# Kernel tuning notes

Measured on AMD Instinct MI355X. Metric: run time of the kernel, lower is better.

The kernel has to match this reference:

```python
import jax, jax.numpy as jnp
import numpy as np

N_USERS = 200000
N_ITEMS = 100000
N_EDGES = 1000000
D = 64
NUM_LAYERS = 3
BATCH = 8192


def setup_inputs() -> dict:
    key = jax.random.key(0)
    ks = jax.random.split(key, 8)
    return {
        "user_feat": jax.random.normal(ks[0], (N_USERS, D), dtype=jnp.float32) * 0.1,
        "item_feat": jax.random.normal(ks[1], (N_ITEMS, D), dtype=jnp.float32) * 0.1,
        "edge_u": jax.random.randint(ks[2], (N_EDGES,), 0, N_USERS, dtype=jnp.int32),
        "edge_i": jax.random.randint(ks[3], (N_EDGES,), 0, N_ITEMS, dtype=jnp.int32),
        "norm": jax.random.uniform(ks[4], (N_EDGES,), dtype=jnp.float32),
        "users": jax.random.randint(ks[5], (BATCH,), 0, N_USERS, dtype=jnp.int32),
        "pos_items": jax.random.randint(ks[6], (BATCH,), 0, N_ITEMS, dtype=jnp.int32),
        "neg_items": jax.random.randint(ks[7], (BATCH,), 0, N_ITEMS, dtype=jnp.int32),
    }


def reference(user_feat, item_feat, edge_u, edge_i, norm, users, pos_items, neg_items):
    # LightGCN propagation: each layer does edge-weighted gather-scatter
    # (u_mul_e 'h','norm' -> sum) in both directions of the bipartite graph.
    u_h, i_h = user_feat, item_feat
    u_acc, i_acc = u_h, i_h
    w = norm[:, None]  # [E, 1]
    for _ in range(NUM_LAYERS):
        # user -> item messages
        new_i = jax.ops.segment_sum(u_h[edge_u] * w, edge_i, num_segments=N_ITEMS)
        # item -> user messages
        new_u = jax.ops.segment_sum(i_h[edge_i] * w, edge_u, num_segments=N_USERS)
        u_h, i_h = new_u, new_i
        u_acc = u_acc + u_h
        i_acc = i_acc + i_h
    scale = 1.0 / (NUM_LAYERS + 1)
    u_acc = u_acc * scale
    i_acc = i_acc * scale
    return (u_acc[users], i_acc[pos_items], i_acc[neg_items])
```

## Files before the change

### kernel.cpp

```cpp
#include <hip/hip_runtime.h>


#define N_USERS 200000
#define N_ITEMS 100000
#define N_EDGES 1000000
#define DIM 64
#define BATCH 8192
#define NTOT (N_USERS + N_ITEMS)
#define NOUT (3 * BATCH)
#define NPART 293
#define PLOCAL 1024

#define HA 489
#define NUNITS (NTOT * DIM / 8)
#define CB ((NUNITS + 1023) / 1024)
#define OB (NOUT * 8 / 256)
#define AB8 (NTOT / 32)
#define FB ((NOUT + 255) / 256)

__device__ __forceinline__ unsigned f2bf(float f) {
    unsigned u = __float_as_uint(f);
    return (u + 0x7fffu + ((u >> 16) & 1u)) >> 16;
}
__device__ __forceinline__ uint2 pack4(float4 v) {
    uint2 o;
    o.x = f2bf(v.x) | (f2bf(v.y) << 16);
    o.y = f2bf(v.z) | (f2bf(v.w) << 16);
    return o;
}
__device__ __forceinline__ void fma4(float4& a, uint2 v, float w) {
    a.x += __uint_as_float(v.x << 16) * w;
    a.y += __uint_as_float(v.x & 0xffff0000u) * w;
    a.z += __uint_as_float(v.y << 16) * w;
    a.w += __uint_as_float(v.y & 0xffff0000u) * w;
}
__device__ __forceinline__ int out_bucket(int orow, const int* users,
                                          const int* pos, const int* neg) {
    int seg = orow >> 13;
    int b = orow & (BATCH - 1);
    if (seg == 0) return users[b];
    if (seg == 1) return N_USERS + pos[b];
    return N_USERS + neg[b];
}

__global__ void hist_kernel(const int* __restrict__ eu,
                            const int* __restrict__ ei,
                            int* __restrict__ partTotals)
{
    __shared__ int lh[NPART];
    int bid = blockIdx.x;
    for (int k = threadIdx.x; k < NPART; k += 256) lh[k] = 0;
    __syncthreads();
    int e0 = (bid * 256 + threadIdx.x) * 8;
    if (e0 < N_EDGES) {
        int4 u0 = *reinterpret_cast<const int4*>(eu + e0);
        int4 u1 = *reinterpret_cast<const int4*>(eu + e0 + 4);
        int4 i0 = *reinterpret_cast<const int4*>(ei + e0);
        int4 i1 = *reinterpret_cast<const int4*>(ei + e0 + 4);
        atomicAdd(&lh[u0.x >> 10], 1);
        atomicAdd(&lh[u0.y >> 10], 1);
        atomicAdd(&lh[u0.z >> 10], 1);
        atomicAdd(&lh[u0.w >> 10], 1);
        atomicAdd(&lh[u1.x >> 10], 1);
        atomicAdd(&lh[u1.y >> 10], 1);
        atomicAdd(&lh[u1.z >> 10], 1);
        atomicAdd(&lh[u1.w >> 10], 1);
        atomicAdd(&lh[(N_USERS + i0.x) >> 10], 1);
        atomicAdd(&lh[(N_USERS + i0.y) >> 10], 1);
        atomicAdd(&lh[(N_USERS + i0.z) >> 10], 1);
        atomicAdd(&lh[(N_USERS + i0.w) >> 10], 1);
        atomicAdd(&lh[(N_USERS + i1.x) >> 10], 1);
        atomicAdd(&lh[(N_USERS + i1.y) >> 10], 1);
        atomicAdd(&lh[(N_USERS + i1.z) >> 10], 1);
        atomicAdd(&lh[(N_USERS + i1.w) >> 10], 1);
    }
    __syncthreads();
    for (int k = threadIdx.x; k < NPART; k += 256) {
        int v = lh[k];
        if (v) atomicAdd(&partTotals[k], v);
    }
}

__global__ void part_scan_kernel(const int* __restrict__ partTotals,
                                 int* __restrict__ partStart,
                                 int* __restrict__ gcur)
{
    __shared__ int s[512];
    int t = threadIdx.x;
    s[t] = (t < NPART) ? partTotals[t] : 0;
    __syncthreads();
    for (int off = 1; off < 512; off <<= 1) {
        int x = (t >= off) ? s[t - off] : 0;
        __syncthreads();
        s[t] += x;
        __syncthreads();
    }
    if (t < NPART) {
        int st = (t == 0) ? 0 : s[t - 1];
        partStart[t] = st;
        gcur[t] = st;
    }
    if (t == NPART) partStart[NPART] = s[NPART - 1];
}

__global__ void partition_conv_kernel(const int* __restrict__ eu,
                                      const int* __restrict__ ei,
                                      const float* __restrict__ w,
                                      int* __restrict__ gcur,
                                      uint2* __restrict__ partBuf,
                                      const float4* __restrict__ uf4,
                                      const float4* __restrict__ if4,
                                      unsigned short* __restrict__ F0,
                                      const float* __restrict__ u_feat,
                                      const float* __restrict__ i_feat,
                                      const int* __restrict__ users,
                                      const int* __restrict__ pos,
                                      const int* __restrict__ neg,
                                      float* __restrict__ out)
{
    int bid = blockIdx.x, t = threadIdx.x;
    if (bid < HA) {
        __shared__ int lh[NPART];
        __shared__ int lcur[NPART];
        for (int k = t; k < NPART; k += 256) lh[k] = 0;
        __syncthreads();
        int e0 = (bid * 256 + t) * 8;
        bool act = e0 < N_EDGES;
        int4 u0, u1, i0, i1;
        if (act) {
            u0 = *reinterpret_cast<const int4*>(eu + e0);
            u1 = *reinterpret_cast<const int4*>(eu + e0 + 4);
            i0 = *reinterpret_cast<const int4*>(ei + e0);
            i1 = *reinterpret_cast<const int4*>(ei + e0 + 4);
            atomicAdd(&lh[u0.x >> 10], 1);
            atomicAdd(&lh[u0.y >> 10], 1);
            atomicAdd(&lh[u0.z >> 10], 1);
            atomicAdd(&lh[u0.w >> 10], 1);
            atomicAdd(&lh[u1.x >> 10], 1);
            atomicAdd(&lh[u1.y >> 10], 1);
            atomicAdd(&lh[u1.z >> 10], 1);
            atomicAdd(&lh[u1.w >> 10], 1);
            atomicAdd(&lh[(N_USERS + i0.x) >> 10], 1);
            atomicAdd(&lh[(N_USERS + i0.y) >> 10], 1);
            atomicAdd(&lh[(N_USERS + i0.z) >> 10], 1);
            atomicAdd(&lh[(N_USERS + i0.w) >> 10], 1);
            atomicAdd(&lh[(N_USERS + i1.x) >> 10], 1);
            atomicAdd(&lh[(N_USERS + i1.y) >> 10], 1);
            atomicAdd(&lh[(N_USERS + i1.z) >> 10], 1);
            atomicAdd(&lh[(N_USERS + i1.w) >> 10], 1);
        }
        __syncthreads();
        for (int k = t; k < NPART; k += 256) {
            int v = lh[k];
            lcur[k] = v ? atomicAdd(&gcur[k], v) : 0;
        }
        __syncthreads();
        if (act) {
            float4 wa = *reinterpret_cast<const float4*>(w + e0);
            float4 wb = *reinterpret_cast<const float4*>(w + e0 + 4);
            int us[8] = {u0.x, u0.y, u0.z, u0.w, u1.x, u1.y, u1.z, u1.w};
            int is[8] = {i0.x, i0.y, i0.z, i0.w, i1.x, i1.y, i1.z, i1.w};
            float ws[8] = {wa.x, wa.y, wa.z, wa.w, wb.x, wb.y, wb.z, wb.w};
            #pragma unroll
            for (int j = 0; j < 8; ++j) {
                int bu = us[j];
                int bi = N_USERS + is[j];
                unsigned wbits = __float_as_uint(ws[j]);
                int su = atomicAdd(&lcur[bu >> 10], 1);
                partBuf[su] = make_uint2((unsigned)(bu & 1023) | ((unsigned)bi << 10), wbits);
                int si = atomicAdd(&lcur[bi >> 10], 1);
                partBuf[si] = make_uint2((unsigned)(bi & 1023) | ((unsigned)bu << 10), wbits);
            }
        }
    } else if (bid < HA + CB) {
        const int NU4 = N_USERS * DIM / 4;
        int jb = (bid - HA) * 1024 + t;
        float4 a[4], b[4];
        #pragma unroll
        for (int c = 0; c < 4; ++c) {
            int j = jb + c * 256;
            if (j < NUNITS) {
                int f4 = j * 2;
                if (f4 < NU4) { a[c] = uf4[f4];       b[c] = uf4[f4 + 1]; }
                else          { a[c] = if4[f4 - NU4]; b[c] = if4[f4 - NU4 + 1]; }
            }
        }
        #pragma unroll
        for (int c = 0; c < 4; ++c) {
            int j = jb + c * 256;
            if (j < NUNITS) {
                uint2 pa = pack4(a[c]), pb = pack4(b[c]);
                *reinterpret_cast<uint4*>(F0 + (size_t)j * 8) =
                    make_uint4(pa.x, pa.y, pb.x, pb.y);
            }
        }
    } else {
        int idx = (bid - HA - CB) * 256 + t;
        int row = idx >> 3;
        if (row >= NOUT) return;
        int d8 = (idx & 7) << 3;
        int seg = row >> 13;
        int b = row & (BATCH - 1);
        const float* src;
        if (seg == 0)      src = u_feat + (size_t)users[b] * DIM;
        else if (seg == 1) src = i_feat + (size_t)pos[b]   * DIM;
        else               src = i_feat + (size_t)neg[b]   * DIM;
        float4 v0 = *reinterpret_cast<const float4*>(src + d8);
        float4 v1 = *reinterpret_cast<const float4*>(src + d8 + 4);
        v0.x *= 0.25f; v0.y *= 0.25f; v0.z *= 0.25f; v0.w *= 0.25f;
        v1.x *= 0.25f; v1.y *= 0.25f; v1.z *= 0.25f; v1.w *= 0.25f;
        float* op = out + (size_t)row * DIM + d8;
        *reinterpret_cast<float4*>(op) = v0;
        *reinterpret_cast<float4*>(op + 4) = v1;
    }
}

__global__ void __launch_bounds__(1024)
build_csr_kernel(const int* __restrict__ partStart,
                 const uint2* __restrict__ partBuf,
                 int* __restrict__ rp,
                 int2* __restrict__ entries)
{
    __shared__ int h[PLOCAL];
    __shared__ int s[PLOCAL];
    __shared__ int cur[PLOCAL];
    int p = blockIdx.x, t = threadIdx.x;
    int base = partStart[p], end = partStart[p + 1];
    h[t] = 0;
    __syncthreads();
    for (int r = base + t; r < end; r += 1024)
        atomicAdd(&h[partBuf[r].x & 1023], 1);
    __syncthreads();
    s[t] = h[t];
    __syncthreads();
    for (int off = 1; off < 1024; off <<= 1) {
        int x = (t >= off) ? s[t - off] : 0;
        __syncthreads();
        s[t] += x;
        __syncthreads();
    }
    int c0 = base + s[t] - h[t];
    cur[t] = c0;
    int gb = p * PLOCAL + t;
    if (gb <= NTOT) rp[gb] = c0;
    __syncthreads();
    for (int r = base + t; r < end; r += 1024) {
        uint2 rec = partBuf[r];
        int slot = atomicAdd(&cur[rec.x & 1023], 1);
        entries[slot] = make_int2((int)(rec.x >> 10), (int)rec.y);
    }
}

__device__ __forceinline__ void agg_row8(int row, int l8, int gb,
                                         const int* __restrict__ rp,
                                         const int2* __restrict__ entries,
                                         const unsigned short* __restrict__ src,
                                         float4& sL, float4& sH)
{
    int beg = rp[row], cnt = rp[row + 1] - beg;
    float4 a0L = {0,0,0,0}, a0H = {0,0,0,0}, a1L = {0,0,0,0}, a1H = {0,0,0,0};
    for (int base = 0; base < cnt; base += 8) {
        int2 e = make_int2(0, 0);
        if (base + l8 < cnt) e = entries[beg + base + l8];
        int   c[8];
        float wv[8];
        #pragma unroll
        for (int k = 0; k < 8; ++k) {
            c[k]  = __shfl(e.x, gb + k);
            wv[k] = __int_as_float(__shfl(e.y, gb + k));
        }
        uint4 v[8];
        #pragma unroll
        for (int k = 0; k < 8; ++k)
            v[k] = *reinterpret_cast<const uint4*>(
                src + (size_t)c[k] * DIM + l8 * 8);
        #pragma unroll
        for (int k = 0; k < 8; ++k) {
            if (k & 1) {
                fma4(a1L, make_uint2(v[k].x, v[k].y), wv[k]);
                fma4(a1H, make_uint2(v[k].z, v[k].w), wv[k]);
            } else {
                fma4(a0L, make_uint2(v[k].x, v[k].y), wv[k]);
                fma4(a0H, make_uint2(v[k].z, v[k].w), wv[k]);
            }
        }
    }
    sL.x = a0L.x + a1L.x; sL.y = a0L.y + a1L.y;
    sL.z = a0L.z + a1L.z; sL.w = a0L.w + a1L.w;
    sH.x = a0H.x + a1H.x; sH.y = a0H.y + a1H.y;
    sH.z = a0H.z + a1H.z; sH.w = a0H.w + a1H.w;
}

__global__ void __launch_bounds__(256, 2)
agg1_flag_kernel(const int* __restrict__ rp,
                 const int2* __restrict__ entries,
                 const unsigned short* __restrict__ F0,
                 unsigned short* __restrict__ H1,
                 const int* __restrict__ users,
                 const int* __restrict__ pos,
                 const int* __restrict__ neg,
                 int* __restrict__ flags)
{
    int bid = blockIdx.x;
    if (bid < AB8) {
        int gid = bid * 256 + threadIdx.x;
        int lane = gid & 63;
        int l8 = lane & 7;
        int gb = lane & 56;
        int row = gid >> 3;
        if (row >= NTOT) return;
        float4 sL, sH;
        agg_row8(row, l8, gb, rp, entries, F0, sL, sH);
        uint2 pL = pack4(sL), pH = pack4(sH);
        *reinterpret_cast<uint4*>(H1 + (size_t)row * DIM + l8 * 8) =
            make_uint4(pL.x, pL.y, pH.x, pH.y);
    } else {
        int t = (bid - AB8) * 256 + threadIdx.x;
        if (t >= NOUT) return;
        int bucket = out_bucket(t, users, pos, neg);
        flags[bucket] = 1;
        int beg = rp[bucket], end = rp[bucket + 1];
        for (int k = beg; k < end; ++k)
            flags[entries[k].x] = 1;
    }
}

__global__ void compact_kernel(const int* __restrict__ flags,
                               int* __restrict__ list,
                               int* __restrict__ count)
{
    int t = blockIdx.x * blockDim.x + threadIdx.x;
    int idx = t * 4;
    if (idx >= NTOT) return;
    int4 f = *reinterpret_cast<const int4*>(flags + idx);
    int loc[4]; int k = 0;
    if (f.x) loc[k++] = idx;
    if (f.y) loc[k++] = idx + 1;
    if (f.z) loc[k++] = idx + 2;
    if (f.w) loc[k++] = idx + 3;
    if (k) {
        int base = atomicAdd(count, k);
        for (int m = 0; m < k; ++m) list[base + m] = loc[m];
    }
}

__global__ void __launch_bounds__(256, 2)
agg2_add1_kernel(const int* __restrict__ rp,
                 const int2* __restrict__ entries,
                 const unsigned short* __restrict__ H1,
                 unsigned short* __restrict__ H2,
                 const int* __restrict__ list,
                 const int* __restrict__ count,
                 const int* __restrict__ users,
                 const int* __restrict__ pos,
                 const int* __restrict__ neg,
                 float* __restrict__ out)
{
    int bid = blockIdx.x;
    if (bid < AB8) {
        int gid = bid * 256 + threadIdx.x;
        int lane = gid & 63;
        int l8 = lane & 7;
        int gb = lane & 56;
        int idx = gid >> 3;
        int n = *count;
        if (idx >= n) return;
        int row = list[idx];
        float4 sL, sH;
        agg_row8(row, l8, gb, rp, entries, H1, sL, sH);
        uint2 pL = pack4(sL), pH = pack4(sH);
        *reinterpret_cast<uint4*>(H2 + (size_t)row * DIM + l8 * 8) =
            make_uint4(pL.x, pL.y, pH.x, pH.y);
    } else {
        int idx = (bid - AB8) * 256 + threadIdx.x;
        int row = idx >> 3;
        if (row >= NOUT) return;
        int d8 = (idx & 7) << 3;
        int bucket = out_bucket(row, users, pos, neg);
        uint4 v = *reinterpret_cast<const uint4*>(H1 + (size_t)bucket * DIM + d8);
        float* op = out + (size_t)row * DIM + d8;
        float4 o0 = *reinterpret_cast<const float4*>(op);
        float4 o1 = *reinterpret_cast<const float4*>(op + 4);
        o0.x += 0.25f * __uint_as_float(v.x << 16);
        o0.y += 0.25f * __uint_as_float(v.x & 0xffff0000u);
        o0.z += 0.25f * __uint_as_float(v.y << 16);
        o0.w += 0.25f * __uint_as_float(v.y & 0xffff0000u);
        o1.x += 0.25f * __uint_as_float(v.z << 16);
        o1.y += 0.25f * __uint_as_float(v.z & 0xffff0000u);
        o1.z += 0.25f * __uint_as_float(v.w << 16);
        o1.w += 0.25f * __uint_as_float(v.w & 0xffff0000u);
        *reinterpret_cast<float4*>(op) = o0;
        *reinterpret_cast<float4*>(op + 4) = o1;
    }
}

__global__ void __launch_bounds__(256, 2)
aggout_add2_kernel(const int* __restrict__ rp,
                   const int2* __restrict__ entries,
                   const unsigned short* __restrict__ H2,
                   const int* __restrict__ users,
                   const int* __restrict__ pos,
                   const int* __restrict__ neg,
                   float* __restrict__ out)
{
    int gid = blockIdx.x * 256 + threadIdx.x;
    int lane = gid & 63;
    int l8 = lane & 7;
    int gb = lane & 56;
    int orow = gid >> 3;
    if (orow >= NOUT) return;
    int bucket = out_bucket(orow, users, pos, neg);
    float4 sL, sH;
    agg_row8(bucket, l8, gb, rp, entries, H2, sL, sH);
    uint4 v = *reinterpret_cast<const uint4*>(H2 + (size_t)bucket * DIM + l8 * 8);
    sL.x += __uint_as_float(v.x << 16);
    sL.y += __uint_as_float(v.x & 0xffff0000u);
    sL.z += __uint_as_float(v.y << 16);
    sL.w += __uint_as_float(v.y & 0xffff0000u);
    sH.x += __uint_as_float(v.z << 16);
    sH.y += __uint_as_float(v.z & 0xffff0000u);
    sH.z += __uint_as_float(v.w << 16);
    sH.w += __uint_as_float(v.w & 0xffff0000u);
    float* op = out + (size_t)orow * DIM + l8 * 8;
    float4 o0 = *reinterpret_cast<const float4*>(op);
    float4 o1 = *reinterpret_cast<const float4*>(op + 4);
    o0.x += 0.25f * sL.x; o0.y += 0.25f * sL.y;
    o0.z += 0.25f * sL.z; o0.w += 0.25f * sL.w;
    o1.x += 0.25f * sH.x; o1.y += 0.25f * sH.y;
    o1.z += 0.25f * sH.z; o1.w += 0.25f * sH.w;
    *reinterpret_cast<float4*>(op) = o0;
    *reinterpret_cast<float4*>(op + 4) = o1;
}

extern "C" void kernel_launch(void* const* d_in, const int* in_sizes, int n_in,
                              void* d_out, int out_size, void* d_ws, size_t ws_size,
                              hipStream_t stream)
{
    const float* user_feat = (const float*)d_in[0];
    const float* item_feat = (const float*)d_in[1];
    const int*   eu        = (const int*)d_in[2];
    const int*   ei        = (const int*)d_in[3];
    const float* norm      = (const float*)d_in[4];
    const int*   users     = (const int*)d_in[5];
    const int*   pos       = (const int*)d_in[6];
    const int*   neg       = (const int*)d_in[7];
    float* out = (float*)d_out;

    auto align256 = [](size_t x) { return (x + 255) & ~(size_t)255; };
    const size_t hBytes = (size_t)NTOT * DIM * sizeof(unsigned short);

    char* p = (char*)d_ws;
    unsigned short* F0 = (unsigned short*)p; p += align256(hBytes);
    unsigned short* H1 = (unsigned short*)p; p += align256(hBytes);
    unsigned short* H2 = (unsigned short*)p; p += align256(hBytes);
    int* partTotals = (int*)p; p += align256((size_t)(512 + NTOT + 16) * 4);
    int* flags = partTotals + 512;
    int* count = flags + NTOT;
    int*  partStart = (int*)p;  p += align256(512 * 4);
    int*  gcur      = (int*)p;  p += align256(512 * 4);
    int*  rp        = (int*)p;  p += align256((size_t)(NTOT + 1) * 4);
    uint2* partBuf  = (uint2*)p; p += align256((size_t)2 * N_EDGES * 8);
    int*  list      = (int*)p;  p += align256((size_t)NTOT * 4);
    int2* entries   = (int2*)p; p += align256((size_t)2 * N_EDGES * 8);

    hipMemsetAsync(partTotals, 0, (size_t)(512 + NTOT + 16) * 4, stream);

    hist_kernel<<<HA, 256, 0, stream>>>(eu, ei, partTotals);

    part_scan_kernel<<<1, 512, 0, stream>>>(partTotals, partStart, gcur);

    partition_conv_kernel<<<HA + CB + OB, 256, 0, stream>>>(
        eu, ei, norm, gcur, partBuf,
        (const float4*)user_feat, (const float4*)item_feat, F0,
        user_feat, item_feat, users, pos, neg, out);

    build_csr_kernel<<<NPART, 1024, 0, stream>>>(partStart, partBuf, rp, entries);

    agg1_flag_kernel<<<AB8 + FB, 256, 0, stream>>>(
        rp, entries, F0, H1, users, pos, neg, flags);

    compact_kernel<<<(NTOT / 4 + 255) / 256, 256, 0, stream>>>(flags, list, count);

    agg2_add1_kernel<<<AB8 + OB, 256, 0, stream>>>(
        rp, entries, H1, H2, list, count, users, pos, neg, out);

    aggout_add2_kernel<<<NOUT / 32, 256, 0, stream>>>(
        rp, entries, H2, users, pos, neg, out);
}
```

Baseline: 284.0 us.

## Replace histogram+scan with fixed-capacity partition buckets and nontemporal stores

Removes the histogram and partition-scan kernels by giving each of the 293 partitions a fixed-capacity slot region (CAP entries) in the partition buffer, so edges are bucketed directly with per-partition counters starting at zero. Row pointers become (start,count) int2 pairs, so each row needs one load instead of two. Streaming outputs (F0, H1, H2, partBuf, entries) now use nontemporal stores to avoid polluting cache, and launch_bounds hints are dropped. The fixed capacity assumes no partition exceeds CAP entries for these inputs, which is a correctness risk for skewed graphs, and it enlarges the workspace footprint.

After: 398.6 us. 1.4x slower.

```diff
diff --git a/kernel.cpp b/kernel.cpp
--- a/kernel.cpp
+++ b/kernel.cpp
@@ -10,6 +10,7 @@
 #define NOUT (3 * BATCH)
 #define NPART 293
 #define PLOCAL 1024
+#define CAP 11264
 
 #define HA 489
 #define NUNITS (NTOT * DIM / 8)
@@ -17,6 +18,10 @@
 #define OB (NOUT * 8 / 256)
 #define AB8 (NTOT / 32)
 #define FB ((NOUT + 255) / 256)
+
+typedef int      int2v  __attribute__((ext_vector_type(2)));
+typedef unsigned uint2v __attribute__((ext_vector_type(2)));
+typedef unsigned uint4v __attribute__((ext_vector_type(4)));
 
 __device__ __forceinline__ unsigned f2bf(float f) {
     unsigned u = __float_as_uint(f);
@@ -41,66 +46,6 @@
     if (seg == 0) return users[b];
     if (seg == 1) return N_USERS + pos[b];
     return N_USERS + neg[b];
-}
-
-__global__ void hist_kernel(const int* __restrict__ eu,
-                            const int* __restrict__ ei,
-                            int* __restrict__ partTotals)
-{
-    __shared__ int lh[NPART];
-    int bid = blockIdx.x;
-    for (int k = threadIdx.x; k < NPART; k += 256) lh[k] = 0;
-    __syncthreads();
-    int e0 = (bid * 256 + threadIdx.x) * 8;
-    if (e0 < N_EDGES) {
-        int4 u0 = *reinterpret_cast<const int4*>(eu + e0);
-        int4 u1 = *reinterpret_cast<const int4*>(eu + e0 + 4);
-        int4 i0 = *reinterpret_cast<const int4*>(ei + e0);
-        int4 i1 = *reinterpret_cast<const int4*>(ei + e0 + 4);
-        atomicAdd(&lh[u0.x >> 10], 1);
-        atomicAdd(&lh[u0.y >> 10], 1);
-        atomicAdd(&lh[u0.z >> 10], 1);
-        atomicAdd(&lh[u0.w >> 10], 1);
-        atomicAdd(&lh[u1.x >> 10], 1);
-        atomicAdd(&lh[u1.y >> 10], 1);
-        atomicAdd(&lh[u1.z >> 10], 1);
-        atomicAdd(&lh[u1.w >> 10], 1);
-        atomicAdd(&lh[(N_USERS + i0.x) >> 10], 1);
-        atomicAdd(&lh[(N_USERS + i0.y) >> 10], 1);
-        atomicAdd(&lh[(N_USERS + i0.z) >> 10], 1);
-        atomicAdd(&lh[(N_USERS + i0.w) >> 10], 1);
-        atomicAdd(&lh[(N_USERS + i1.x) >> 10], 1);
-        atomicAdd(&lh[(N_USERS + i1.y) >> 10], 1);
-        atomicAdd(&lh[(N_USERS + i1.z) >> 10], 1);
-        atomicAdd(&lh[(N_USERS + i1.w) >> 10], 1);
-    }
-    __syncthreads();
-    for (int k = threadIdx.x; k < NPART; k += 256) {
-        int v = lh[k];
-        if (v) atomicAdd(&partTotals[k], v);
-    }
-}
-
-__global__ void part_scan_kernel(const int* __restrict__ partTotals,
-                                 int* __restrict__ partStart,
-                                 int* __restrict__ gcur)
-{
-    __shared__ int s[512];
-    int t = threadIdx.x;
-    s[t] = (t < NPART) ? partTotals[t] : 0;
-    __syncthreads();
-    for (int off = 1; off < 512; off <<= 1) {
-        int x = (t >= off) ? s[t - off] : 0;
-        __syncthreads();
-        s[t] += x;
-        __syncthreads();
-    }
-    if (t < NPART) {
-        int st = (t == 0) ? 0 : s[t - 1];
-        partStart[t] = st;
-        gcur[t] = st;
-    }
-    if (t == NPART) partStart[NPART] = s[NPART - 1];
 }
 
 __global__ void partition_conv_kernel(const int* __restrict__ eu,
@@ -166,10 +111,15 @@
                 int bu = us[j];
                 int bi = N_USERS + is[j];
                 unsigned wbits = __float_as_uint(ws[j]);
-                int su = atomicAdd(&lcur[bu >> 10], 1);
-                partBuf[su] = make_uint2((unsigned)(bu & 1023) | ((unsigned)bi << 10), wbits);
-                int si = atomicAdd(&lcur[bi >> 10], 1);
-                partBuf[si] = make_uint2((unsigned)(bi & 1023) | ((unsigned)bu << 10), wbits);
+                int pu = bu >> 10, pi = bi >> 10;
+                int su = atomicAdd(&lcur[pu], 1);
+                uint2v ru = {(unsigned)(bu & 1023) | ((unsigned)bi << 10), wbits};
+                __builtin_nontemporal_store(ru,
+                    (uint2v*)&partBuf[(size_t)pu * CAP + su]);
+                int si = atomicAdd(&lcur[pi], 1);
+                uint2v ri = {(unsigned)(bi & 1023) | ((unsigned)bu << 10), wbits};
+                __builtin_nontemporal_store(ri,
+                    (uint2v*)&partBuf[(size_t)pi * CAP + si]);
             }
         }
     } else if (bid < HA + CB) {
@@ -190,8 +140,8 @@
             int j = jb + c * 256;
             if (j < NUNITS) {
                 uint2 pa = pack4(a[c]), pb = pack4(b[c]);
-                *reinterpret_cast<uint4*>(F0 + (size_t)j * 8) =
-                    make_uint4(pa.x, pa.y, pb.x, pb.y);
+                uint4v o = {pa.x, pa.y, pb.x, pb.y};
+                __builtin_nontemporal_store(o, (uint4v*)(F0 + (size_t)j * 8));
             }
         }
     } else {
@@ -216,16 +166,17 @@
 }
 
 __global__ void __launch_bounds__(1024)
-build_csr_kernel(const int* __restrict__ partStart,
+build_csr_kernel(const int* __restrict__ gcur,
                  const uint2* __restrict__ partBuf,
-                 int* __restrict__ rp,
+                 int2* __restrict__ rp2,
                  int2* __restrict__ entries)
 {
     __shared__ int h[PLOCAL];
     __shared__ int s[PLOCAL];
     __shared__ int cur[PLOCAL];
     int p = blockIdx.x, t = threadIdx.x;
-    int base = partStart[p], end = partStart[p + 1];
+    int base = p * CAP;
+    int end = base + gcur[p];
     h[t] = 0;
     __syncthreads();
     for (int r = base + t; r < end; r += 1024)
@@ -242,22 +193,22 @@
     int c0 = base + s[t] - h[t];
     cur[t] = c0;
     int gb = p * PLOCAL + t;
-    if (gb <= NTOT) rp[gb] = c0;
+    if (gb < NTOT) rp2[gb] = make_int2(c0, h[t]);
     __syncthreads();
     for (int r = base + t; r < end; r += 1024) {
         uint2 rec = partBuf[r];
         int slot = atomicAdd(&cur[rec.x & 1023], 1);
-        entries[slot] = make_int2((int)(rec.x >> 10), (int)rec.y);
-    }
-}
-
-__device__ __forceinline__ void agg_row8(int row, int l8, int gb,
-                                         const int* __restrict__ rp,
+        int2v e = {(int)(rec.x >> 10), (int)rec.y};
+        __builtin_nontemporal_store(e, (int2v*)&entries[slot]);
+    }
+}
+
+__device__ __forceinline__ void agg_row8(int2 rc, int l8, int gb,
                                          const int2* __restrict__ entries,
                                          const unsigned short* __restrict__ src,
                                          float4& sL, float4& sH)
 {
-    int beg = rp[row], cnt = rp[row + 1] - beg;
+    int beg = rc.x, cnt = rc.y;
     float4 a0L = {0,0,0,0}, a0H = {0,0,0,0}, a1L = {0,0,0,0}, a1H = {0,0,0,0};
     for (int base = 0; base < cnt; base += 8) {
         int2 e = make_int2(0, 0);
@@ -291,15 +242,14 @@
     sH.z = a0H.z + a1H.z; sH.w = a0H.w + a1H.w;
 }
 
-__global__ void __launch_bounds__(256, 2)
-agg1_flag_kernel(const int* __restrict__ rp,
-                 const int2* __restrict__ entries,
-                 const unsigned short* __restrict__ F0,
-                 unsigned short* __restrict__ H1,
-                 const int* __restrict__ users,
-                 const int* __restrict__ pos,
-                 const int* __restrict__ neg,
-                 int* __restrict__ flags)
+__global__ void agg1_flag_kernel(const int2* __restrict__ rp2,
+                                 const int2* __restrict__ entries,
+                                 const unsigned short* __restrict__ F0,
+                                 unsigned short* __restrict__ H1,
+                                 const int* __restrict__ users,
+                                 const int* __restrict__ pos,
+                                 const int* __restrict__ neg,
+                                 int* __restrict__ flags)
 {
     int bid = blockIdx.x;
     if (bid < AB8) {
@@ -310,17 +260,17 @@
         int row = gid >> 3;
         if (row >= NTOT) return;
         float4 sL, sH;
-        agg_row8(row, l8, gb, rp, entries, F0, sL, sH);
+        agg_row8(rp2[row], l8, gb, entries, F0, sL, sH);
         uint2 pL = pack4(sL), pH = pack4(sH);
-        *reinterpret_cast<uint4*>(H1 + (size_t)row * DIM + l8 * 8) =
-            make_uint4(pL.x, pL.y, pH.x, pH.y);
+        uint4v o = {pL.x, pL.y, pH.x, pH.y};
+        __builtin_nontemporal_store(o, (uint4v*)(H1 + (size_t)row * DIM + l8 * 8));
     } else {
         int t = (bid - AB8) * 256 + threadIdx.x;
         if (t >= NOUT) return;
         int bucket = out_bucket(t, users, pos, neg);
         flags[bucket] = 1;
-        int beg = rp[bucket], end = rp[bucket + 1];
-        for (int k = beg; k < end; ++k)
+        int2 rc = rp2[bucket];
+        for (int k = rc.x; k < rc.x + rc.y; ++k)
             flags[entries[k].x] = 1;
     }
 }
@@ -344,17 +294,16 @@
     }
 }
 
-__global__ void __launch_bounds__(256, 2)
-agg2_add1_kernel(const int* __restrict__ rp,
-                 const int2* __restrict__ entries,
-                 const unsigned short* __restrict__ H1,
-                 unsigned short* __restrict__ H2,
-                 const int* __restrict__ list,
-                 const int* __restrict__ count,
-                 const int* __restrict__ users,
-                 const int* __restrict__ pos,
-                 const int* __restrict__ neg,
-                 float* __restrict__ out)
+__global__ void agg2_add1_kernel(const int2* __restrict__ rp2,
+                                 const int2* __restrict__ entries,
+                                 const unsigned short* __restrict__ H1,
+                                 unsigned short* __restrict__ H2,
+                                 const int* __restrict__ list,
+                                 const int* __restrict__ count,
+                                 const int* __restrict__ users,
+                                 const int* __restrict__ pos,
+                                 const int* __restrict__ neg,
+                                 float* __restrict__ out)
 {
     int bid = blockIdx.x;
     if (bid < AB8) {
@@ -367,10 +316,10 @@
         if (idx >= n) return;
         int row = list[idx];
         float4 sL, sH;
-        agg_row8(row, l8, gb, rp, entries, H1, sL, sH);
+        agg_row8(rp2[row], l8, gb, entries, H1, sL, sH);
         uint2 pL = pack4(sL), pH = pack4(sH);
-        *reinterpret_cast<uint4*>(H2 + (size_t)row * DIM + l8 * 8) =
-            make_uint4(pL.x, pL.y, pH.x, pH.y);
+        uint4v o = {pL.x, pL.y, pH.x, pH.y};
+        __builtin_nontemporal_store(o, (uint4v*)(H2 + (size_t)row * DIM + l8 * 8));
     } else {
         int idx = (bid - AB8) * 256 + threadIdx.x;
         int row = idx >> 3;
@@ -394,14 +343,13 @@
     }
 }
 
-__global__ void __launch_bounds__(256, 2)
-aggout_add2_kernel(const int* __restrict__ rp,
-                   const int2* __restrict__ entries,
-                   const unsigned short* __restrict__ H2,
-                   const int* __restrict__ users,
-                   const int* __restrict__ pos,
-                   const int* __restrict__ neg,
-                   float* __restrict__ out)
+__global__ void aggout_add2_kernel(const int2* __restrict__ rp2,
+                                   const int2* __restrict__ entries,
+                                   const unsigned short* __restrict__ H2,
+                                   const int* __restrict__ users,
+                                   const int* __restrict__ pos,
+                                   const int* __restrict__ neg,
+                                   float* __restrict__ out)
 {
     int gid = blockIdx.x * 256 + threadIdx.x;
     int lane = gid & 63;
@@ -411,7 +359,7 @@
     if (orow >= NOUT) return;
     int bucket = out_bucket(orow, users, pos, neg);
     float4 sL, sH;
-    agg_row8(bucket, l8, gb, rp, entries, H2, sL, sH);
+    agg_row8(rp2[bucket], l8, gb, entries, H2, sL, sH);
     uint4 v = *reinterpret_cast<const uint4*>(H2 + (size_t)bucket * DIM + l8 * 8);
     sL.x += __uint_as_float(v.x << 16);
     sL.y += __uint_as_float(v.x & 0xffff0000u);
@@ -448,42 +396,37 @@
 
     auto align256 = [](size_t x) { return (x + 255) & ~(size_t)255; };
     const size_t hBytes = (size_t)NTOT * DIM * sizeof(unsigned short);
+    const size_t pBytes = (size_t)NPART * CAP * 8;
 
     char* p = (char*)d_ws;
     unsigned short* F0 = (unsigned short*)p; p += align256(hBytes);
     unsigned short* H1 = (unsigned short*)p; p += align256(hBytes);
     unsigned short* H2 = (unsigned short*)p; p += align256(hBytes);
-    int* partTotals = (int*)p; p += align256((size_t)(512 + NTOT + 16) * 4);
-    int* flags = partTotals + 512;
+    int* gcur = (int*)p; p += align256((size_t)(512 + NTOT + 16) * 4);
+    int* flags = gcur + 512;
     int* count = flags + NTOT;
-    int*  partStart = (int*)p;  p += align256(512 * 4);
-    int*  gcur      = (int*)p;  p += align256(512 * 4);
-    int*  rp        = (int*)p;  p += align256((size_t)(NTOT + 1) * 4);
-    uint2* partBuf  = (uint2*)p; p += align256((size_t)2 * N_EDGES * 8);
-    int*  list      = (int*)p;  p += align256((size_t)NTOT * 4);
-    int2* entries   = (int2*)p; p += align256((size_t)2 * N_EDGES * 8);
-
-    hipMemsetAsync(partTotals, 0, (size_t)(512 + NTOT + 16) * 4, stream);
-
-    hist_kernel<<<HA, 256, 0, stream>>>(eu, ei, partTotals);
-
-    part_scan_kernel<<<1, 512, 0, stream>>>(partTotals, partStart, gcur);
+    int2* rp2      = (int2*)p;  p += align256((size_t)NTOT * 8);
+    uint2* partBuf = (uint2*)p; p += align256(pBytes);
+    int*  list     = (int*)p;   p += align256((size_t)NTOT * 4);
+    int2* entries  = (int2*)p;  p += align256(pBytes);
+
+    hipMemsetAsync(gcur, 0, (size_t)(512 + NTOT + 16) * 4, stream);
 
     partition_conv_kernel<<<HA + CB + OB, 256, 0, stream>>>(
         eu, ei, norm, gcur, partBuf,
         (const float4*)user_feat, (const float4*)item_feat, F0,
         user_feat, item_feat, users, pos, neg, out);
 
-    build_csr_kernel<<<NPART, 1024, 0, stream>>>(partStart, partBuf, rp, entries);
+    build_csr_kernel<<<NPART, 1024, 0, stream>>>(gcur, partBuf, rp2, entries);
 
     agg1_flag_kernel<<<AB8 + FB, 256, 0, stream>>>(
-        rp, entries, F0, H1, users, pos, neg, flags);
+        rp2, entries, F0, H1, users, pos, neg, flags);
 
     compact_kernel<<<(NTOT / 4 + 255) / 256, 256, 0, stream>>>(flags, list, count);
 
     agg2_add1_kernel<<<AB8 + OB, 256, 0, stream>>>(
-        rp, entries, H1, H2, list, count, users, pos, neg, out);
+        rp2, entries, H1, H2, list, count, users, pos, neg, out);
 
     aggout_add2_kernel<<<NOUT / 32, 256, 0, stream>>>(
-        rp, entries, H2, users, pos, neg, out);
-}
+        rp2, entries, H2, users, pos, neg, out);
+}
```
